# Kernel tuning notes

Hardware: AMD Instinct MI355X
Metric: run time of the kernel (lower is better)

## Reference

```python
import jax, jax.numpy as jnp
import numpy as np

D = 512
H = 8
HD = D // H
EPS = 1e-5
NEG_INF = -1e30


def _ln(x, g, b):
    mu = jnp.mean(x, axis=-1, keepdims=True)
    var = jnp.mean(jnp.square(x - mu), axis=-1, keepdims=True)
    return (x - mu) * jax.lax.rsqrt(var + EPS) * g + b


def setup_inputs() -> dict:
    key = jax.random.key(0)
    ks = jax.random.split(key, 8)
    V, M, S = 128, 128, 514  # seq includes 2 head tokens (cls+dist)
    inp = {
        "video_embeds": jax.random.normal(ks[0], (V, D), jnp.float32),
        "music_features": jax.random.normal(ks[1], (M, S, D), jnp.float32),
        "music_masks": jnp.ones((M, S - 2), jnp.int32),
    }
    wk = jax.random.split(ks[2], 5)
    for name, k in zip(["Wq", "Wk", "Wv", "Wo", "Wl"], wk):
        inp[name] = jax.random.normal(k, (D, D), jnp.float32) * 0.02
    for name in ["bq", "bk", "bv", "bo", "bl"]:
        inp[name] = jnp.zeros((D,), jnp.float32)
    for name in ["g1", "g2", "g3"]:
        inp[name] = jnp.ones((D,), jnp.float32)
    for name in ["b1", "b2", "b3"]:
        inp[name] = jnp.zeros((D,), jnp.float32)
    return inp


def reference(video_embeds, music_features, music_masks,
              Wq, bq, Wk, bk, Wv, bv, Wo, bo, Wl, bl,
              g1, b1, g2, b2, g3, b3):
    # drop cls + dist tokens
    mf = music_features[:, 2:, :]  # (M, f, D)
    ve = _ln(video_embeds, g1, b1)  # (V, D)
    mf = _ln(mf, g1, b1)
    V = ve.shape[0]
    M, f, _ = mf.shape

    q = (ve @ Wq.T + bq).reshape(V, H, HD).transpose(1, 0, 2)        # (H, V, hd)
    k = (mf @ Wk.T + bk).reshape(M, f, H, HD).transpose(0, 2, 1, 3)  # (M, H, f, hd)
    v = (mf @ Wv.T + bv).reshape(M, f, H, HD).transpose(0, 2, 1, 3)  # (M, H, f, hd)

    logits = jnp.einsum('hvd,mhfd->vmhf', q, k) / np.sqrt(HD).astype(np.float32)
    mask = music_masks[None, :, None, :]  # (1, M, 1, f)
    logits = jnp.where(mask == 0, NEG_INF, logits)
    w = jax.nn.softmax(logits, axis=-1)
    attn = jnp.einsum('vmhf,mhfd->vmhd', w, v).reshape(V, M, D)
    attn = attn @ Wo.T + bo

    attn = _ln(attn, g2, b2)
    out = attn + (attn @ Wl.T + bl)  # dropout = identity in eval
    return _ln(out, g3, b3)
```

## Files before the change

### kernel.cpp

```cpp
#include <hip/hip_runtime.h>
#include <hip/hip_bf16.h>

typedef unsigned int uint;
typedef unsigned short ushort;
typedef __bf16 bf16;
typedef bf16 bf16x8 __attribute__((ext_vector_type(8)));
typedef float f32x4 __attribute__((ext_vector_type(4)));
typedef ushort ushort4v __attribute__((ext_vector_type(4)));

__device__ __forceinline__ float bf2f(ushort u) {
  union { uint u; float f; } v; v.u = ((uint)u) << 16; return v.f;
}
__device__ __forceinline__ ushort f2bf(float f) {
  union { float f; uint u; } v; v.f = f;
  uint u = v.u;
  uint r = (u + 0x7fffu + ((u >> 16) & 1u)) >> 16;
  return (ushort)r;
}

__device__ __forceinline__ void gl2lds16(const void* g, void* l) {
  __builtin_amdgcn_global_load_lds(
      (const __attribute__((address_space(1))) void*)g,
      (__attribute__((address_space(3))) void*)l, 16, 0, 0);
}

__device__ __forceinline__ void ln_rows0(
    int nrows, int blk, int nblk, int tid,
    const float* __restrict__ srcA,
    const float* __restrict__ g, const float* __restrict__ b,
    ushort* __restrict__ dst)
{
  const int l = tid & 63;
  const int nw = nblk * 4;
  for (int row = blk * 4 + (tid >> 6); row < nrows; row += nw) {
    const float* s = srcA + (size_t)row * 512;
    float x[8];
    float4 a0 = *(const float4*)(s + l * 4);
    float4 a1 = *(const float4*)(s + 256 + l * 4);
    x[0] = a0.x; x[1] = a0.y; x[2] = a0.z; x[3] = a0.w;
    x[4] = a1.x; x[5] = a1.y; x[6] = a1.z; x[7] = a1.w;
    float sum = 0.f, sq = 0.f;
    #pragma unroll
    for (int j = 0; j < 8; ++j) { sum += x[j]; sq += x[j] * x[j]; }
    #pragma unroll
    for (int o = 1; o < 64; o <<= 1) {
      sum += __shfl_xor(sum, o);
      sq  += __shfl_xor(sq, o);
    }
    float mu = sum * (1.f / 512.f);
    float var = sq * (1.f / 512.f) - mu * mu;
    float rstd = rsqrtf(var + 1e-5f);
    float4 g0 = *(const float4*)(g + l * 4);
    float4 g1 = *(const float4*)(g + 256 + l * 4);
    float4 b0 = *(const float4*)(b + l * 4);
    float4 b1 = *(const float4*)(b + 256 + l * 4);
    float gv[8] = {g0.x,g0.y,g0.z,g0.w,g1.x,g1.y,g1.z,g1.w};
    float bv[8] = {b0.x,b0.y,b0.z,b0.w,b1.x,b1.y,b1.z,b1.w};
    ushort* d = dst + (size_t)row * 512;
    ushort4v p0, p1;
    #pragma unroll
    for (int j = 0; j < 4; ++j) {
      p0[j] = f2bf((x[j] - mu) * rstd * gv[j] + bv[j]);
      p1[j] = f2bf((x[4+j] - mu) * rstd * gv[4+j] + bv[4+j]);
    }
    *(ushort4v*)(d + l * 4) = p0;
    *(ushort4v*)(d + 256 + l * 4) = p1;
  }
}

__device__ __forceinline__ void ln_pair(
    int mode, int wid, int tid,
    const void* __restrict__ srcA, const void* __restrict__ srcB,
    const float* __restrict__ g, const float* __restrict__ b,
    void* __restrict__ dst)
{
  const int l = tid & 63;
  const int r0 = wid * 2, r1 = r0 + 1;
  float x0[8], x1[8];
  if (mode == 1) {
    int mm0 = r0 >> 9, fi0 = r0 & 511;
    int mm1 = r1 >> 9, fi1 = r1 & 511;
    const float* s0 = (const float*)srcA + ((size_t)mm0 * 514 + 2 + fi0) * 512;
    const float* s1 = (const float*)srcA + ((size_t)mm1 * 514 + 2 + fi1) * 512;
    float4 a0 = *(const float4*)(s0 + l * 4);
    float4 a1 = *(const float4*)(s0 + 256 + l * 4);
    float4 c0 = *(const float4*)(s1 + l * 4);
    float4 c1 = *(const float4*)(s1 + 256 + l * 4);
    x0[0]=a0.x; x0[1]=a0.y; x0[2]=a0.z; x0[3]=a0.w;
    x0[4]=a1.x; x0[5]=a1.y; x0[6]=a1.z; x0[7]=a1.w;
    x1[0]=c0.x; x1[1]=c0.y; x1[2]=c0.z; x1[3]=c0.w;
    x1[4]=c1.x; x1[5]=c1.y; x1[6]=c1.z; x1[7]=c1.w;
  } else if (mode == 2) {
    const ushort* s0 = (const ushort*)srcA + (size_t)r0 * 512;
    const ushort* s1 = (const ushort*)srcA + (size_t)r1 * 512;
    uint4 u0 = *(const uint4*)(s0 + l * 8);
    uint4 u1 = *(const uint4*)(s1 + l * 8);
    x0[0]=bf2f((ushort)u0.x); x0[1]=bf2f((ushort)(u0.x>>16));
    x0[2]=bf2f((ushort)u0.y); x0[3]=bf2f((ushort)(u0.y>>16));
    x0[4]=bf2f((ushort)u0.z); x0[5]=bf2f((ushort)(u0.z>>16));
    x0[6]=bf2f((ushort)u0.w); x0[7]=bf2f((ushort)(u0.w>>16));
    x1[0]=bf2f((ushort)u1.x); x1[1]=bf2f((ushort)(u1.x>>16));
    x1[2]=bf2f((ushort)u1.y); x1[3]=bf2f((ushort)(u1.y>>16));
    x1[4]=bf2f((ushort)u1.z); x1[5]=bf2f((ushort)(u1.z>>16));
    x1[6]=bf2f((ushort)u1.w); x1[7]=bf2f((ushort)(u1.w>>16));
  } else {
    const ushort* sa0 = (const ushort*)srcA + (size_t)r0 * 512;
    const ushort* sb0 = (const ushort*)srcB + (size_t)r0 * 512;
    const ushort* sa1 = (const ushort*)srcA + (size_t)r1 * 512;
    const ushort* sb1 = (const ushort*)srcB + (size_t)r1 * 512;
    uint4 ua0 = *(const uint4*)(sa0 + l * 8);
    uint4 ub0 = *(const uint4*)(sb0 + l * 8);
    uint4 ua1 = *(const uint4*)(sa1 + l * 8);
    uint4 ub1 = *(const uint4*)(sb1 + l * 8);
    x0[0]=bf2f((ushort)ua0.x)+bf2f((ushort)ub0.x);
    x0[1]=bf2f((ushort)(ua0.x>>16))+bf2f((ushort)(ub0.x>>16));
    x0[2]=bf2f((ushort)ua0.y)+bf2f((ushort)ub0.y);
    x0[3]=bf2f((ushort)(ua0.y>>16))+bf2f((ushort)(ub0.y>>16));
    x0[4]=bf2f((ushort)ua0.z)+bf2f((ushort)ub0.z);
    x0[5]=bf2f((ushort)(ua0.z>>16))+bf2f((ushort)(ub0.z>>16));
    x0[6]=bf2f((ushort)ua0.w)+bf2f((ushort)ub0.w);
    x0[7]=bf2f((ushort)(ua0.w>>16))+bf2f((ushort)(ub0.w>>16));
    x1[0]=bf2f((ushort)ua1.x)+bf2f((ushort)ub1.x);
    x1[1]=bf2f((ushort)(ua1.x>>16))+bf2f((ushort)(ub1.x>>16));
    x1[2]=bf2f((ushort)ua1.y)+bf2f((ushort)ub1.y);
    x1[3]=bf2f((ushort)(ua1.y>>16))+bf2f((ushort)(ub1.y>>16));
    x1[4]=bf2f((ushort)ua1.z)+bf2f((ushort)ub1.z);
    x1[5]=bf2f((ushort)(ua1.z>>16))+bf2f((ushort)(ub1.z>>16));
    x1[6]=bf2f((ushort)ua1.w)+bf2f((ushort)ub1.w);
    x1[7]=bf2f((ushort)(ua1.w>>16))+bf2f((ushort)(ub1.w>>16));
  }
  float s0 = 0.f, q0 = 0.f, s1 = 0.f, q1 = 0.f;
  #pragma unroll
  for (int j = 0; j < 8; ++j) {
    s0 += x0[j]; q0 += x0[j] * x0[j];
    s1 += x1[j]; q1 += x1[j] * x1[j];
  }
  #pragma unroll
  for (int o = 1; o < 64; o <<= 1) {
    s0 += __shfl_xor(s0, o); q0 += __shfl_xor(q0, o);
    s1 += __shfl_xor(s1, o); q1 += __shfl_xor(q1, o);
  }
  float mu0 = s0 * (1.f/512.f), mu1 = s1 * (1.f/512.f);
  float rstd0 = rsqrtf(q0 * (1.f/512.f) - mu0 * mu0 + 1e-5f);
  float rstd1 = rsqrtf(q1 * (1.f/512.f) - mu1 * mu1 + 1e-5f);

  float gv[8], bv[8];
  if (mode == 1) {
    float4 g0 = *(const float4*)(g + l * 4);
    float4 g1v = *(const float4*)(g + 256 + l * 4);
    float4 b0 = *(const float4*)(b + l * 4);
    float4 b1v = *(const float4*)(b + 256 + l * 4);
    gv[0]=g0.x; gv[1]=g0.y; gv[2]=g0.z; gv[3]=g0.w;
    gv[4]=g1v.x; gv[5]=g1v.y; gv[6]=g1v.z; gv[7]=g1v.w;
    bv[0]=b0.x; bv[1]=b0.y; bv[2]=b0.z; bv[3]=b0.w;
    bv[4]=b1v.x; bv[5]=b1v.y; bv[6]=b1v.z; bv[7]=b1v.w;
  } else {
    float4 g0 = *(const float4*)(g + l * 8);
    float4 g1v = *(const float4*)(g + l * 8 + 4);
    float4 b0 = *(const float4*)(b + l * 8);
    float4 b1v = *(const float4*)(b + l * 8 + 4);
    gv[0]=g0.x; gv[1]=g0.y; gv[2]=g0.z; gv[3]=g0.w;
    gv[4]=g1v.x; gv[5]=g1v.y; gv[6]=g1v.z; gv[7]=g1v.w;
    bv[0]=b0.x; bv[1]=b0.y; bv[2]=b0.z; bv[3]=b0.w;
    bv[4]=b1v.x; bv[5]=b1v.y; bv[6]=b1v.z; bv[7]=b1v.w;
  }
  if (mode == 1) {
    ushort* d0 = (ushort*)dst + (size_t)r0 * 512;
    ushort* d1 = (ushort*)dst + (size_t)r1 * 512;
    ushort4v p00, p01, p10, p11;
    #pragma unroll
    for (int j = 0; j < 4; ++j) {
      p00[j] = f2bf((x0[j]-mu0)*rstd0*gv[j]+bv[j]);
      p01[j] = f2bf((x0[4+j]-mu0)*rstd0*gv[4+j]+bv[4+j]);
      p10[j] = f2bf((x1[j]-mu1)*rstd1*gv[j]+bv[j]);
      p11[j] = f2bf((x1[4+j]-mu1)*rstd1*gv[4+j]+bv[4+j]);
    }
    *(ushort4v*)(d0 + l * 4) = p00;
    *(ushort4v*)(d0 + 256 + l * 4) = p01;
    *(ushort4v*)(d1 + l * 4) = p10;
    *(ushort4v*)(d1 + 256 + l * 4) = p11;
  } else if (mode == 2) {
    ushort* d0 = (ushort*)dst + (size_t)r0 * 512;
    ushort* d1 = (ushort*)dst + (size_t)r1 * 512;
    uint4 o0, o1;
    float y;
    uint t;
    y = (x0[0]-mu0)*rstd0*gv[0]+bv[0]; t = f2bf(y);
    o0.x = t | ((uint)f2bf((x0[1]-mu0)*rstd0*gv[1]+bv[1]) << 16);
    o0.y = (uint)f2bf((x0[2]-mu0)*rstd0*gv[2]+bv[2]) | ((uint)f2bf((x0[3]-mu0)*rstd0*gv[3]+bv[3]) << 16);
    o0.z = (uint)f2bf((x0[4]-mu0)*rstd0*gv[4]+bv[4]) | ((uint)f2bf((x0[5]-mu0)*rstd0*gv[5]+bv[5]) << 16);
    o0.w = (uint)f2bf((x0[6]-mu0)*rstd0*gv[6]+bv[6]) | ((uint)f2bf((x0[7]-mu0)*rstd0*gv[7]+bv[7]) << 16);
    o1.x = (uint)f2bf((x1[0]-mu1)*rstd1*gv[0]+bv[0]) | ((uint)f2bf((x1[1]-mu1)*rstd1*gv[1]+bv[1]) << 16);
    o1.y = (uint)f2bf((x1[2]-mu1)*rstd1*gv[2]+bv[2]) | ((uint)f2bf((x1[3]-mu1)*rstd1*gv[3]+bv[3]) << 16);
    o1.z = (uint)f2bf((x1[4]-mu1)*rstd1*gv[4]+bv[4]) | ((uint)f2bf((x1[5]-mu1)*rstd1*gv[5]+bv[5]) << 16);
    o1.w = (uint)f2bf((x1[6]-mu1)*rstd1*gv[6]+bv[6]) | ((uint)f2bf((x1[7]-mu1)*rstd1*gv[7]+bv[7]) << 16);
    *(uint4*)(d0 + l * 8) = o0;
    *(uint4*)(d1 + l * 8) = o1;
  } else {
    float* d0 = (float*)dst + (size_t)r0 * 512;
    float* d1 = (float*)dst + (size_t)r1 * 512;
    float4 a0, a1, c0, c1;
    a0.x=(x0[0]-mu0)*rstd0*gv[0]+bv[0]; a0.y=(x0[1]-mu0)*rstd0*gv[1]+bv[1];
    a0.z=(x0[2]-mu0)*rstd0*gv[2]+bv[2]; a0.w=(x0[3]-mu0)*rstd0*gv[3]+bv[3];
    a1.x=(x0[4]-mu0)*rstd0*gv[4]+bv[4]; a1.y=(x0[5]-mu0)*rstd0*gv[5]+bv[5];
    a1.z=(x0[6]-mu0)*rstd0*gv[6]+bv[6]; a1.w=(x0[7]-mu0)*rstd0*gv[7]+bv[7];
    c0.x=(x1[0]-mu1)*rstd1*gv[0]+bv[0]; c0.y=(x1[1]-mu1)*rstd1*gv[1]+bv[1];
    c0.z=(x1[2]-mu1)*rstd1*gv[2]+bv[2]; c0.w=(x1[3]-mu1)*rstd1*gv[3]+bv[3];
    c1.x=(x1[4]-mu1)*rstd1*gv[4]+bv[4]; c1.y=(x1[5]-mu1)*rstd1*gv[5]+bv[5];
    c1.z=(x1[6]-mu1)*rstd1*gv[6]+bv[6]; c1.w=(x1[7]-mu1)*rstd1*gv[7]+bv[7];
    *(float4*)(d0 + l * 8) = a0;
    *(float4*)(d0 + l * 8 + 4) = a1;
    *(float4*)(d1 + l * 8) = c0;
    *(float4*)(d1 + l * 8 + 4) = c1;
  }
}

__global__ __launch_bounds__(256) void ln512p(
    int mode, const void* __restrict__ srcA, const void* __restrict__ srcB,
    const float* __restrict__ g, const float* __restrict__ b,
    void* __restrict__ dst)
{
  ln_pair(mode, blockIdx.x * 4 + (threadIdx.x >> 6), threadIdx.x, srcA, srcB, g, b, dst);
}

struct PreArgs {
  const float* s0; const float* s1; const float* s2; const float* s3; const float* s4;
  ushort* d0; ushort* d1; ushort* d2; ushort* d3; ushort* d4;
  const float* video; const float* music;
  const float* g1; const float* b1;
  ushort* veln; ushort* mfln;
};
__global__ __launch_bounds__(256) void preamble(PreArgs a) {
  int bb = blockIdx.x;
  if (bb < 640) {
    int t = bb * 256 + threadIdx.x;
    int which = t >> 15;
    int e = (t & 32767) * 8;
    const float* s = which == 0 ? a.s0 : which == 1 ? a.s1 : which == 2 ? a.s2 : which == 3 ? a.s3 : a.s4;
    ushort*      d = which == 0 ? a.d0 : which == 1 ? a.d1 : which == 2 ? a.d2 : which == 3 ? a.d3 : a.d4;
    float4 v0 = *(const float4*)(s + e);
    float4 v1 = *(const float4*)(s + e + 4);
    uint4 o;
    o.x = (uint)f2bf(v0.x) | ((uint)f2bf(v0.y) << 16);
    o.y = (uint)f2bf(v0.z) | ((uint)f2bf(v0.w) << 16);
    o.z = (uint)f2bf(v1.x) | ((uint)f2bf(v1.y) << 16);
    o.w = (uint)f2bf(v1.z) | ((uint)f2bf(v1.w) << 16);
    *(uint4*)(d + e) = o;
  } else if (bb < 672) {
    ln_rows0(128, bb - 640, 32, threadIdx.x, a.video, a.g1, a.b1, a.veln);
  } else {
    ln_pair(1, (bb - 672) * 4 + (threadIdx.x >> 6), threadIdx.x,
            a.music, nullptr, a.g1, a.b1, a.mfln);
  }
}

__global__ __launch_bounds__(256) void gemm_t3(
    const ushort* __restrict__ A, const ushort* __restrict__ W,
    const float* __restrict__ bias, ushort* __restrict__ C,
    float scale, int vt_mode,
    const ushort* __restrict__ Aq, const ushort* __restrict__ Wqp,
    const float* __restrict__ bqp, ushort* __restrict__ Qout, int qy)
{
  __shared__ __align__(16) ushort As[2][128 * 64];
  __shared__ __align__(16) ushort Bs[2][128 * 64];
  const int tid = threadIdx.x;
  const int w = tid >> 6, l = tid & 63;
  const int lg = l >> 4, lr = l & 15;
  const int wr = w >> 1, wc = w & 1;

  int row0, col0;
  const bool isq = ((int)blockIdx.y == qy);
  if (isq) {
    A = Aq; W = Wqp; bias = bqp; C = Qout; scale = 0.125f; vt_mode = 0;
    row0 = 0; col0 = blockIdx.x * 128;
  } else {
    int nwg = gridDim.x * (qy >= 0 ? qy : gridDim.y);
    int bid = blockIdx.y * gridDim.x + blockIdx.x;
    if ((nwg & 7) == 0) bid = (bid & 7) * (nwg >> 3) + (bid >> 3);
    row0 = (bid / gridDim.x) * 128;
    col0 = (bid % gridDim.x) * 128;
  }

  f32x4 acc[4][4];
  #pragma unroll
  for (int i = 0; i < 4; i++)
    #pragma unroll
    for (int j = 0; j < 4; j++) { f32x4 z = {0.f,0.f,0.f,0.f}; acc[i][j] = z; }

  size_t asrc[4], wsrc[4]; int ldst[4];
  #pragma unroll
  for (int c2 = 0; c2 < 4; ++c2) {
    int c = c2 * 256 + tid;
    int r = c >> 3, j = c & 7;
    int koff = (j ^ (r & 7)) * 8;
    asrc[c2] = (size_t)(row0 + r) * 512 + koff;
    wsrc[c2] = (size_t)(col0 + r) * 512 + koff;
    ldst[c2] = (c2 * 256 + w * 64) * 8;
  }

  auto stage = [&](int pb, int kk) {
    #pragma unroll
    for (int c2 = 0; c2 < 4; ++c2) {
      gl2lds16(A + asrc[c2] + kk * 64, &As[pb][ldst[c2]]);
      gl2lds16(W + wsrc[c2] + kk * 64, &Bs[pb][ldst[c2]]);
    }
  };
  auto compute = [&](int pb) {
    #pragma unroll
    for (int ks = 0; ks < 2; ++ks) {
      bf16x8 af[4], bfr[4];
      #pragma unroll
      for (int mi = 0; mi < 4; ++mi) {
        int r = wr * 64 + mi * 16 + lr;
        af[mi] = *(const bf16x8*)(&As[pb][r * 64 + ((ks * 32 + lg * 8) ^ ((r & 7) * 8))]);
      }
      #pragma unroll
      for (int ni = 0; ni < 4; ++ni) {
        int r = wc * 64 + ni * 16 + lr;
        bfr[ni] = *(const bf16x8*)(&Bs[pb][r * 64 + ((ks * 32 + lg * 8) ^ ((r & 7) * 8))]);
      }
      #pragma unroll
      for (int mi = 0; mi < 4; ++mi)
        #pragma unroll
        for (int ni = 0; ni < 4; ++ni)
          acc[mi][ni] = __builtin_amdgcn_mfma_f32_16x16x32_bf16(af[mi], bfr[ni], acc[mi][ni], 0, 0, 0);
    }
  };

  stage(0, 0);
  __syncthreads();
  int cur = 0;
  #pragma unroll
  for (int kk = 0; kk < 7; ++kk) {
    stage(cur ^ 1, kk + 1);
    compute(cur);
    __syncthreads();
    cur ^= 1;
  }
  compute(cur);
  __syncthreads();

  ushort* img = (ushort*)As;
  #pragma unroll
  for (int ni = 0; ni < 4; ++ni) {
    float bc = bias[col0 + wc * 64 + ni * 16 + lr];
    #pragma unroll
    for (int mi = 0; mi < 4; ++mi) {
      #pragma unroll
      for (int e = 0; e < 4; ++e) {
        float v = (acc[mi][ni][e] + bc) * scale;
        int x, y;
        if (!vt_mode) { x = wr * 64 + mi * 16 + lg * 4 + e; y = wc * 64 + ni * 16 + lr; }
        else          { x = wc * 64 + ni * 16 + lr;         y = wr * 64 + mi * 16 + lg * 4 + e; }
        int byte = x * 256 + ((y * 2) ^ (((x >> 2) & 3) * 32));
        img[byte >> 1] = f2bf(v);
      }
    }
  }
  __syncthreads();
  {
    const int m = row0 >> 9, fi0 = row0 & 511;
    #pragma unroll
    for (int pass = 0; pass < 8; ++pass) {
      int r = pass * 16 + (tid >> 4);
      int cb = tid & 15;
      int byte = r * 256 + ((cb * 16) ^ (((r >> 2) & 3) * 32));
      uint4 d = *(const uint4*)(img + (byte >> 1));
      if (!vt_mode)
        *(uint4*)(C + (size_t)(row0 + r) * 512 + col0 + cb * 8) = d;
      else
        *(uint4*)(C + (size_t)(m * 512 + col0 + r) * 512 + fi0 + cb * 8) = d;
    }
  }
}

__global__ __launch_bounds__(256) void attn_kernel(
    const ushort* __restrict__ q, const ushort* __restrict__ k,
    const ushort* __restrict__ vt, const int* __restrict__ masks,
    ushort* __restrict__ attn)
{
  __shared__ __align__(16) ushort Qs[128 * 64];
  __shared__ __align__(16) ushort Ks[64 * 64];
  __shared__ __align__(16) ushort Vs[64 * 64];
  __shared__ __align__(16) ushort Ps[4][32 * 64];
  __shared__ float maskf[64];
  __shared__ float stats[4][32];

  const int tid = threadIdx.x;
  const int w = tid >> 6, l = tid & 63;
  const int lg = l >> 4, lr = l & 15;
  const int m = blockIdx.x >> 3, h = blockIdx.x & 7;

  const size_t kbase = (size_t)(m * 512) * 512 + h * 64;
  const size_t vbase = (size_t)(m * 512 + h * 64) * 512;

  #pragma unroll
  for (int c2 = 0; c2 < 4; ++c2) {
    int c = c2 * 256 + tid;
    int r = c >> 3, j = c & 7;
    gl2lds16(q + (size_t)r * 512 + h * 64 + ((j * 8) ^ ((r & 7) * 8)),
             Qs + (c2 * 256 + w * 64) * 8);
  }

  f32x4 acc[2][4];
  #pragma unroll
  for (int i = 0; i < 2; i++)
    #pragma unroll
    for (int j = 0; j < 4; j++) { f32x4 z = {0.f,0.f,0.f,0.f}; acc[i][j] = z; }
  float m_run[2] = {-INFINITY, -INFINITY};
  float l_run[2] = {0.f, 0.f};
  bf16x8 qf[2][2];

  for (int it = 0; it < 8; ++it) {
    const int f0 = it * 64;
    #pragma unroll
    for (int c2 = 0; c2 < 2; ++c2) {
      int c = c2 * 256 + tid;
      int r = c >> 3, j = c & 7;
      int off = (j * 8) ^ ((r & 7) * 8);
      gl2lds16(k + kbase + (size_t)(f0 + r) * 512 + off, Ks + (c2 * 256 + w * 64) * 8);
      gl2lds16(vt + vbase + (size_t)r * 512 + f0 + off, Vs + (c2 * 256 + w * 64) * 8);
    }
    if (tid < 64) maskf[tid] = masks[m * 512 + f0 + tid] ? 0.f : -1e30f;
    __syncthreads();

    if (it == 0) {
      #pragma unroll
      for (int nv = 0; nv < 2; ++nv)
        #pragma unroll
        for (int k2 = 0; k2 < 2; ++k2) {
          int v = w * 32 + nv * 16 + lr;
          qf[nv][k2] = *(const bf16x8*)(Qs + v * 64 + ((k2 * 32 + lg * 8) ^ ((v & 7) * 8)));
        }
    }

    f32x4 s[4][2];
    #pragma unroll
    for (int mi = 0; mi < 4; mi++)
      #pragma unroll
      for (int nv = 0; nv < 2; nv++) { f32x4 z = {0.f,0.f,0.f,0.f}; s[mi][nv] = z; }
    #pragma unroll
    for (int k2 = 0; k2 < 2; ++k2) {
      bf16x8 kf[4];
      #pragma unroll
      for (int mi = 0; mi < 4; ++mi) {
        int f = mi * 16 + lr;
        kf[mi] = *(const bf16x8*)(Ks + f * 64 + ((k2 * 32 + lg * 8) ^ ((f & 7) * 8)));
      }
      __builtin_amdgcn_s_setprio(1);
      #pragma unroll
      for (int mi = 0; mi < 4; ++mi)
        #pragma unroll
        for (int nv = 0; nv < 2; ++nv)
          s[mi][nv] = __builtin_amdgcn_mfma_f32_16x16x32_bf16(kf[mi], qf[nv][k2], s[mi][nv], 0, 0, 0);
      __builtin_amdgcn_s_setprio(0);
    }

    float mk[4][4];
    #pragma unroll
    for (int mi = 0; mi < 4; mi++)
      #pragma unroll
      for (int e = 0; e < 4; e++) mk[mi][e] = maskf[mi * 16 + lg * 4 + e];

    #pragma unroll
    for (int nv = 0; nv < 2; ++nv) {
      float cmax = -INFINITY;
      #pragma unroll
      for (int mi = 0; mi < 4; mi++)
        #pragma unroll
        for (int e = 0; e < 4; e++) {
          s[mi][nv][e] += mk[mi][e];
          cmax = fmaxf(cmax, s[mi][nv][e]);
        }
      cmax = fmaxf(cmax, __shfl_xor(cmax, 16));
      cmax = fmaxf(cmax, __shfl_xor(cmax, 32));
      float mnew = fmaxf(m_run[nv], cmax);
      float sc = __expf(m_run[nv] - mnew);
      float csum = 0.f;
      int vloc = nv * 16 + lr;
      #pragma unroll
      for (int mi = 0; mi < 4; mi++) {
        ushort4v pk;
        #pragma unroll
        for (int e = 0; e < 4; e++) {
          float p = __expf(s[mi][nv][e] - mnew);
          csum += p;
          pk[e] = f2bf(p);
        }
        int f = mi * 16 + lg * 4;
        *(ushort4v*)(&Ps[w][vloc * 64 + (f ^ ((vloc & 7) * 8))]) = pk;
      }
      csum += __shfl_xor(csum, 16);
      csum += __shfl_xor(csum, 32);
      l_run[nv] = l_run[nv] * sc + csum;
      m_run[nv] = mnew;
      if (lg == 0) stats[w][vloc] = sc;
    }

    #pragma unroll
    for (int mi2 = 0; mi2 < 2; ++mi2)
      #pragma unroll
      for (int e = 0; e < 4; ++e) {
        float sc = stats[w][mi2 * 16 + lg * 4 + e];
        #pragma unroll
        for (int nd = 0; nd < 4; ++nd) acc[mi2][nd][e] *= sc;
      }

    #pragma unroll
    for (int k2 = 0; k2 < 2; ++k2) {
      bf16x8 pf[2], vf[4];
      #pragma unroll
      for (int mi2 = 0; mi2 < 2; ++mi2) {
        int vloc = mi2 * 16 + lr;
        pf[mi2] = *(const bf16x8*)(&Ps[w][vloc * 64 + ((k2 * 32 + lg * 8) ^ ((vloc & 7) * 8))]);
      }
      #pragma unroll
      for (int nd = 0; nd < 4; ++nd) {
        int d = nd * 16 + lr;
        vf[nd] = *(const bf16x8*)(Vs + d * 64 + ((k2 * 32 + lg * 8) ^ ((d & 7) * 8)));
      }
      __builtin_amdgcn_s_setprio(1);
      #pragma unroll
      for (int mi2 = 0; mi2 < 2; ++mi2)
        #pragma unroll
        for (int nd = 0; nd < 4; ++nd)
          acc[mi2][nd] = __builtin_amdgcn_mfma_f32_16x16x32_bf16(pf[mi2], vf[nd], acc[mi2][nd], 0, 0, 0);
      __builtin_amdgcn_s_setprio(0);
    }
    __syncthreads();
  }

  #pragma unroll
  for (int nv = 0; nv < 2; ++nv)
    if (lg == 0) stats[w][nv * 16 + lr] = 1.f / l_run[nv];
  #pragma unroll
  for (int mi2 = 0; mi2 < 2; ++mi2)
    #pragma unroll
    for (int e = 0; e < 4; ++e) {
      float invl = stats[w][mi2 * 16 + lg * 4 + e];
      int vg = w * 32 + mi2 * 16 + lg * 4 + e;
      #pragma unroll
      for (int nd = 0; nd < 4; ++nd) {
        int d = nd * 16 + lr;
        attn[(size_t)(vg * 128 + m) * 512 + h * 64 + d] = f2bf(acc[mi2][nd][e] * invl);
      }
    }
}

extern "C" void kernel_launch(void* const* d_in, const int* in_sizes, int n_in,
                              void* d_out, int out_size, void* d_ws, size_t ws_size,
                              hipStream_t stream) {
  const float* video = (const float*)d_in[0];
  const float* music = (const float*)d_in[1];
  const int*   masks = (const int*)d_in[2];
  const float* Wq = (const float*)d_in[3];
  const float* Wk = (const float*)d_in[4];
  const float* Wv = (const float*)d_in[5];
  const float* Wo = (const float*)d_in[6];
  const float* Wl = (const float*)d_in[7];
  const float* bq = (const float*)d_in[8];
  const float* bk = (const float*)d_in[9];
  const float* bv = (const float*)d_in[10];
  const float* bo = (const float*)d_in[11];
  const float* bl = (const float*)d_in[12];
  const float* g1 = (const float*)d_in[13];
  const float* g2 = (const float*)d_in[14];
  const float* g3 = (const float*)d_in[15];
  const float* b1 = (const float*)d_in[16];
  const float* b2 = (const float*)d_in[17];
  const float* b3 = (const float*)d_in[18];

  char* ws = (char*)d_ws;
  ushort* mfln = (ushort*)(ws);
  ushort* kbuf = (ushort*)(ws + 67108864);
  ushort* vtb  = (ushort*)(ws + 134217728);
  ushort* attn = (ushort*)(ws + 201326592);
  ushort* c1   = (ushort*)(ws + 218103808);
  ushort* xbuf = (ushort*)(ws + 234881024);
  ushort* veln = (ushort*)(ws + 251658240);
  ushort* qbuf = (ushort*)(ws + 251789312);
  ushort* wqb  = (ushort*)(ws + 251920384);
  ushort* wkb  = wqb + 262144;
  ushort* wvb  = wkb + 262144;
  ushort* wob  = wvb + 262144;
  ushort* wlb  = wob + 262144;

  PreArgs pa = {Wq, Wk, Wv, Wo, Wl, wqb, wkb, wvb, wob, wlb,
                video, music, g1, b1, veln, mfln};
  preamble<<<8864, 256, 0, stream>>>(pa);

  gemm_t3<<<dim3(4, 513), 256, 0, stream>>>(
      mfln, wkb, bk, kbuf, 1.f, 0, veln, wqb, bq, qbuf, 512);
  gemm_t3<<<dim3(4, 512), 256, 0, stream>>>(
      mfln, wvb, bv, vtb, 1.f, 1, nullptr, nullptr, nullptr, nullptr, -1);

  attn_kernel<<<1024, 256, 0, stream>>>(qbuf, kbuf, vtb, masks, attn);

  gemm_t3<<<dim3(4, 128), 256, 0, stream>>>(
      attn, wob, bo, c1, 1.f, 0, nullptr, nullptr, nullptr, nullptr, -1);
  ln512p<<<2048, 256, 0, stream>>>(2, c1, nullptr, g2, b2, xbuf);
  gemm_t3<<<dim3(4, 128), 256, 0, stream>>>(
      xbuf, wlb, bl, c1, 1.f, 0, nullptr, nullptr, nullptr, nullptr, -1);
  ln512p<<<2048, 256, 0, stream>>>(3, xbuf, c1, g3, b3, d_out);
}
```

Before: 328.8 us.

## Rework GEMM into 256x128 triple-buffered tiles and double-buffer attention K/V

The GEMM kernel becomes 512-thread blocks with 256x128 tiles, a three-stage LDS ring buffer driven by explicit vmcnt waits, and MFMA priority hints. The LDS-staged epilogue is dropped in favour of direct global stores, and Q projection is split into its own launch. The attention kernel double-buffers K/V/mask loads so the next tile is prefetched during compute, and it skips the running-max rescale when the new max is within a threshold of the old one. The trade-offs are more LDS per block (lower occupancy), less coalesced direct stores, and an extra kernel launch.

```diff
diff --git a/kernel.cpp b/kernel.cpp
--- a/kernel.cpp
+++ b/kernel.cpp
@@ -183,10 +183,7 @@
     ushort* d0 = (ushort*)dst + (size_t)r0 * 512;
     ushort* d1 = (ushort*)dst + (size_t)r1 * 512;
     uint4 o0, o1;
-    float y;
-    uint t;
-    y = (x0[0]-mu0)*rstd0*gv[0]+bv[0]; t = f2bf(y);
-    o0.x = t | ((uint)f2bf((x0[1]-mu0)*rstd0*gv[1]+bv[1]) << 16);
+    o0.x = (uint)f2bf((x0[0]-mu0)*rstd0*gv[0]+bv[0]) | ((uint)f2bf((x0[1]-mu0)*rstd0*gv[1]+bv[1]) << 16);
     o0.y = (uint)f2bf((x0[2]-mu0)*rstd0*gv[2]+bv[2]) | ((uint)f2bf((x0[3]-mu0)*rstd0*gv[3]+bv[3]) << 16);
     o0.z = (uint)f2bf((x0[4]-mu0)*rstd0*gv[4]+bv[4]) | ((uint)f2bf((x0[5]-mu0)*rstd0*gv[5]+bv[5]) << 16);
     o0.w = (uint)f2bf((x0[6]-mu0)*rstd0*gv[6]+bv[6]) | ((uint)f2bf((x0[7]-mu0)*rstd0*gv[7]+bv[7]) << 16);
@@ -254,32 +251,23 @@
   }
 }
 
-__global__ __launch_bounds__(256) void gemm_t3(
+__global__ __launch_bounds__(512) void gemm_p3(
     const ushort* __restrict__ A, const ushort* __restrict__ W,
     const float* __restrict__ bias, ushort* __restrict__ C,
-    float scale, int vt_mode,
-    const ushort* __restrict__ Aq, const ushort* __restrict__ Wqp,
-    const float* __restrict__ bqp, ushort* __restrict__ Qout, int qy)
+    float scale, int vt_mode, int rowlim)
 {
-  __shared__ __align__(16) ushort As[2][128 * 64];
-  __shared__ __align__(16) ushort Bs[2][128 * 64];
+  __shared__ __align__(16) ushort As[3][256 * 64];
+  __shared__ __align__(16) ushort Bs[3][128 * 64];
   const int tid = threadIdx.x;
   const int w = tid >> 6, l = tid & 63;
   const int lg = l >> 4, lr = l & 15;
   const int wr = w >> 1, wc = w & 1;
 
-  int row0, col0;
-  const bool isq = ((int)blockIdx.y == qy);
-  if (isq) {
-    A = Aq; W = Wqp; bias = bqp; C = Qout; scale = 0.125f; vt_mode = 0;
-    row0 = 0; col0 = blockIdx.x * 128;
-  } else {
-    int nwg = gridDim.x * (qy >= 0 ? qy : gridDim.y);
-    int bid = blockIdx.y * gridDim.x + blockIdx.x;
-    if ((nwg & 7) == 0) bid = (bid & 7) * (nwg >> 3) + (bid >> 3);
-    row0 = (bid / gridDim.x) * 128;
-    col0 = (bid % gridDim.x) * 128;
-  }
+  int nwg = gridDim.x * gridDim.y;
+  int bid = blockIdx.y * gridDim.x + blockIdx.x;
+  if ((nwg & 7) == 0) bid = (bid & 7) * (nwg >> 3) + (bid >> 3);
+  const int bx = bid % gridDim.x, by = bid / gridDim.x;
+  const int row0 = by * 256, col0 = bx * 128;
 
   f32x4 acc[4][4];
   #pragma unroll
@@ -287,23 +275,29 @@
     #pragma unroll
     for (int j = 0; j < 4; j++) { f32x4 z = {0.f,0.f,0.f,0.f}; acc[i][j] = z; }
 
-  size_t asrc[4], wsrc[4]; int ldst[4];
-  #pragma unroll
-  for (int c2 = 0; c2 < 4; ++c2) {
-    int c = c2 * 256 + tid;
-    int r = c >> 3, j = c & 7;
+  size_t asrc[4], wsrc[2]; int aldst[4], wldst[2];
+  {
+    int r = tid >> 3, j = tid & 7;
     int koff = (j ^ (r & 7)) * 8;
-    asrc[c2] = (size_t)(row0 + r) * 512 + koff;
-    wsrc[c2] = (size_t)(col0 + r) * 512 + koff;
-    ldst[c2] = (c2 * 256 + w * 64) * 8;
+    #pragma unroll
+    for (int c2 = 0; c2 < 4; ++c2) {
+      asrc[c2] = (size_t)(row0 + c2 * 64 + r) * 512 + koff;
+      aldst[c2] = ((c2 * 64 + w * 8) * 64);
+    }
+    #pragma unroll
+    for (int c2 = 0; c2 < 2; ++c2) {
+      wsrc[c2] = (size_t)(col0 + c2 * 64 + r) * 512 + koff;
+      wldst[c2] = ((c2 * 64 + w * 8) * 64);
+    }
   }
 
   auto stage = [&](int pb, int kk) {
     #pragma unroll
-    for (int c2 = 0; c2 < 4; ++c2) {
-      gl2lds16(A + asrc[c2] + kk * 64, &As[pb][ldst[c2]]);
-      gl2lds16(W + wsrc[c2] + kk * 64, &Bs[pb][ldst[c2]]);
-    }
+    for (int c2 = 0; c2 < 4; ++c2)
+      gl2lds16(A + asrc[c2] + kk * 64, &As[pb][aldst[c2]]);
+    #pragma unroll
+    for (int c2 = 0; c2 < 2; ++c2)
+      gl2lds16(W + wsrc[c2] + kk * 64, &Bs[pb][wldst[c2]]);
   };
   auto compute = [&](int pb) {
     #pragma unroll
@@ -319,57 +313,53 @@
         int r = wc * 64 + ni * 16 + lr;
         bfr[ni] = *(const bf16x8*)(&Bs[pb][r * 64 + ((ks * 32 + lg * 8) ^ ((r & 7) * 8))]);
       }
+      __builtin_amdgcn_s_setprio(1);
       #pragma unroll
       for (int mi = 0; mi < 4; ++mi)
         #pragma unroll
         for (int ni = 0; ni < 4; ++ni)
           acc[mi][ni] = __builtin_amdgcn_mfma_f32_16x16x32_bf16(af[mi], bfr[ni], acc[mi][ni], 0, 0, 0);
+      __builtin_amdgcn_s_setprio(0);
     }
   };
 
   stage(0, 0);
-  __syncthreads();
-  int cur = 0;
-  #pragma unroll
-  for (int kk = 0; kk < 7; ++kk) {
-    stage(cur ^ 1, kk + 1);
-    compute(cur);
-    __syncthreads();
-    cur ^= 1;
-  }
-  compute(cur);
-  __syncthreads();
-
-  ushort* img = (ushort*)As;
+  stage(1, 1);
+  int cb = 0;
+  for (int t = 0; t < 8; ++t) {
+    if (t < 7) asm volatile("s_waitcnt vmcnt(6)" ::: "memory");
+    else       asm volatile("s_waitcnt vmcnt(0)" ::: "memory");
+    __builtin_amdgcn_s_barrier();
+    __builtin_amdgcn_sched_barrier(0);
+    if (t + 2 < 8) {
+      int nb = cb + 2; if (nb >= 3) nb -= 3;
+      stage(nb, t + 2);
+    }
+    compute(cb);
+    cb = (cb == 2) ? 0 : cb + 1;
+  }
+
   #pragma unroll
   for (int ni = 0; ni < 4; ++ni) {
-    float bc = bias[col0 + wc * 64 + ni * 16 + lr];
+    int cg = col0 + wc * 64 + ni * 16 + lr;
+    float bc = bias[cg];
     #pragma unroll
     for (int mi = 0; mi < 4; ++mi) {
-      #pragma unroll
-      for (int e = 0; e < 4; ++e) {
-        float v = (acc[mi][ni][e] + bc) * scale;
-        int x, y;
-        if (!vt_mode) { x = wr * 64 + mi * 16 + lg * 4 + e; y = wc * 64 + ni * 16 + lr; }
-        else          { x = wc * 64 + ni * 16 + lr;         y = wr * 64 + mi * 16 + lg * 4 + e; }
-        int byte = x * 256 + ((y * 2) ^ (((x >> 2) & 3) * 32));
-        img[byte >> 1] = f2bf(v);
-      }
-    }
-  }
-  __syncthreads();
-  {
-    const int m = row0 >> 9, fi0 = row0 & 511;
-    #pragma unroll
-    for (int pass = 0; pass < 8; ++pass) {
-      int r = pass * 16 + (tid >> 4);
-      int cb = tid & 15;
-      int byte = r * 256 + ((cb * 16) ^ (((r >> 2) & 3) * 32));
-      uint4 d = *(const uint4*)(img + (byte >> 1));
-      if (!vt_mode)
-        *(uint4*)(C + (size_t)(row0 + r) * 512 + col0 + cb * 8) = d;
-      else
-        *(uint4*)(C + (size_t)(m * 512 + col0 + r) * 512 + fi0 + cb * 8) = d;
+      int rg0 = row0 + wr * 64 + mi * 16 + lg * 4;
+      if (rg0 >= rowlim) continue;
+      if (!vt_mode) {
+        #pragma unroll
+        for (int e = 0; e < 4; ++e) {
+          float v = (acc[mi][ni][e] + bc) * scale;
+          C[(size_t)(rg0 + e) * 512 + cg] = f2bf(v);
+        }
+      } else {
+        int m = rg0 >> 9, fi = rg0 & 511;
+        ushort4v pk;
+        #pragma unroll
+        for (int e = 0; e < 4; ++e) pk[e] = f2bf((acc[mi][ni][e] + bc) * scale);
+        *(ushort4v*)(C + (size_t)(m * 512 + cg) * 512 + fi) = pk;
+      }
     }
   }
 }
@@ -380,10 +370,10 @@
     ushort* __restrict__ attn)
 {
   __shared__ __align__(16) ushort Qs[128 * 64];
-  __shared__ __align__(16) ushort Ks[64 * 64];
-  __shared__ __align__(16) ushort Vs[64 * 64];
+  __shared__ __align__(16) ushort Ks[2][64 * 64];
+  __shared__ __align__(16) ushort Vs[2][64 * 64];
   __shared__ __align__(16) ushort Ps[4][32 * 64];
-  __shared__ float maskf[64];
+  __shared__ float maskf[2][64];
   __shared__ float stats[4][32];
 
   const int tid = threadIdx.x;
@@ -393,6 +383,19 @@
 
   const size_t kbase = (size_t)(m * 512) * 512 + h * 64;
   const size_t vbase = (size_t)(m * 512 + h * 64) * 512;
+
+  auto stageKV = [&](int pb, int it) {
+    const int f0 = it * 64;
+    #pragma unroll
+    for (int c2 = 0; c2 < 2; ++c2) {
+      int c = c2 * 256 + tid;
+      int r = c >> 3, j = c & 7;
+      int off = (j * 8) ^ ((r & 7) * 8);
+      gl2lds16(k + kbase + (size_t)(f0 + r) * 512 + off, &Ks[pb][(c2 * 256 + w * 64) * 8]);
+      gl2lds16(vt + vbase + (size_t)r * 512 + f0 + off, &Vs[pb][(c2 * 256 + w * 64) * 8]);
+    }
+    if (tid < 64) maskf[pb][tid] = masks[m * 512 + f0 + tid] ? 0.f : -1e30f;
+  };
 
   #pragma unroll
   for (int c2 = 0; c2 < 4; ++c2) {
@@ -401,6 +404,8 @@
     gl2lds16(q + (size_t)r * 512 + h * 64 + ((j * 8) ^ ((r & 7) * 8)),
              Qs + (c2 * 256 + w * 64) * 8);
   }
+  stageKV(0, 0);
+  __syncthreads();
 
   f32x4 acc[2][4];
   #pragma unroll
@@ -410,29 +415,17 @@
   float m_run[2] = {-INFINITY, -INFINITY};
   float l_run[2] = {0.f, 0.f};
   bf16x8 qf[2][2];
-
+  #pragma unroll
+  for (int nv = 0; nv < 2; ++nv)
+    #pragma unroll
+    for (int k2 = 0; k2 < 2; ++k2) {
+      int v = w * 32 + nv * 16 + lr;
+      qf[nv][k2] = *(const bf16x8*)(Qs + v * 64 + ((k2 * 32 + lg * 8) ^ ((v & 7) * 8)));
+    }
+
+  int cur = 0;
   for (int it = 0; it < 8; ++it) {
-    const int f0 = it * 64;
-    #pragma unroll
-    for (int c2 = 0; c2 < 2; ++c2) {
-      int c = c2 * 256 + tid;
-      int r = c >> 3, j = c & 7;
-      int off = (j * 8) ^ ((r & 7) * 8);
-      gl2lds16(k + kbase + (size_t)(f0 + r) * 512 + off, Ks + (c2 * 256 + w * 64) * 8);
-      gl2lds16(vt + vbase + (size_t)r * 512 + f0 + off, Vs + (c2 * 256 + w * 64) * 8);
-    }
-    if (tid < 64) maskf[tid] = masks[m * 512 + f0 + tid] ? 0.f : -1e30f;
-    __syncthreads();
-
-    if (it == 0) {
-      #pragma unroll
-      for (int nv = 0; nv < 2; ++nv)
-        #pragma unroll
-        for (int k2 = 0; k2 < 2; ++k2) {
-          int v = w * 32 + nv * 16 + lr;
-          qf[nv][k2] = *(const bf16x8*)(Qs + v * 64 + ((k2 * 32 + lg * 8) ^ ((v & 7) * 8)));
-        }
-    }
+    if (it < 7) stageKV(cur ^ 1, it + 1);
 
     f32x4 s[4][2];
     #pragma unroll
@@ -445,7 +438,7 @@
       #pragma unroll
       for (int mi = 0; mi < 4; ++mi) {
         int f = mi * 16 + lr;
-        kf[mi] = *(const bf16x8*)(Ks + f * 64 + ((k2 * 32 + lg * 8) ^ ((f & 7) * 8)));
+        kf[mi] = *(const bf16x8*)(&Ks[cur][f * 64 + ((k2 * 32 + lg * 8) ^ ((f & 7) * 8))]);
       }
       __builtin_amdgcn_s_setprio(1);
       #pragma unroll
@@ -460,22 +453,23 @@
     #pragma unroll
     for (int mi = 0; mi < 4; mi++)
       #pragma unroll
-      for (int e = 0; e < 4; e++) mk[mi][e] = maskf[mi * 16 + lg * 4 + e];
+      for (int e = 0; e < 4; e++) mk[mi][e] = maskf[cur][mi * 16 + lg * 4 + e];
 
     #pragma unroll
     for (int nv = 0; nv < 2; ++nv) {
-      float cmax = -INFINITY;
+      float pmax = -INFINITY;
       #pragma unroll
       for (int mi = 0; mi < 4; mi++)
         #pragma unroll
         for (int e = 0; e < 4; e++) {
           s[mi][nv][e] += mk[mi][e];
-          cmax = fmaxf(cmax, s[mi][nv][e]);
+          pmax = fmaxf(pmax, s[mi][nv][e]);
         }
-      cmax = fmaxf(cmax, __shfl_xor(cmax, 16));
-      cmax = fmaxf(cmax, __shfl_xor(cmax, 32));
-      float mnew = fmaxf(m_run[nv], cmax);
-      float sc = __expf(m_run[nv] - mnew);
+      pmax = fmaxf(pmax, __shfl_xor(pmax, 16));
+      pmax = fmaxf(pmax, __shfl_xor(pmax, 32));
+      bool skip = __all(pmax - m_run[nv] <= 8.f);
+      float mnew = skip ? m_run[nv] : fmaxf(m_run[nv], pmax);
+      float sc = skip ? 1.f : __expf(m_run[nv] - mnew);
       float csum = 0.f;
       int vloc = nv * 16 + lr;
       #pragma unroll
@@ -495,16 +489,16 @@
       l_run[nv] = l_run[nv] * sc + csum;
       m_run[nv] = mnew;
       if (lg == 0) stats[w][vloc] = sc;
-    }
-
-    #pragma unroll
-    for (int mi2 = 0; mi2 < 2; ++mi2)
-      #pragma unroll
-      for (int e = 0; e < 4; ++e) {
-        float sc = stats[w][mi2 * 16 + lg * 4 + e];
-        #pragma unroll
-        for (int nd = 0; nd < 4; ++nd) acc[mi2][nd][e] *= sc;
-      }
+      if (!skip) {
+        int mi2 = nv;
+        #pragma unroll
+        for (int e = 0; e < 4; ++e) {
+          float scv = stats[w][mi2 * 16 + lg * 4 + e];
+          #pragma unroll
+          for (int nd = 0; nd < 4; ++nd) acc[mi2][nd][e] *= scv;
+        }
+      }
+    }
 
     #pragma unroll
     for (int k2 = 0; k2 < 2; ++k2) {
@@ -517,7 +511,7 @@
       #pragma unroll
       for (int nd = 0; nd < 4; ++nd) {
         int d = nd * 16 + lr;
-        vf[nd] = *(const bf16x8*)(Vs + d * 64 + ((k2 * 32 + lg * 8) ^ ((d & 7) * 8)));
+        vf[nd] = *(const bf16x8*)(&Vs[cur][d * 64 + ((k2 * 32 + lg * 8) ^ ((d & 7) * 8))]);
       }
       __builtin_amdgcn_s_setprio(1);
       #pragma unroll
@@ -528,6 +522,7 @@
       __builtin_amdgcn_s_setprio(0);
     }
     __syncthreads();
+    cur ^= 1;
   }
 
   #pragma unroll
@@ -589,17 +584,14 @@
                 video, music, g1, b1, veln, mfln};
   preamble<<<8864, 256, 0, stream>>>(pa);
 
-  gemm_t3<<<dim3(4, 513), 256, 0, stream>>>(
-      mfln, wkb, bk, kbuf, 1.f, 0, veln, wqb, bq, qbuf, 512);
-  gemm_t3<<<dim3(4, 512), 256, 0, stream>>>(
-      mfln, wvb, bv, vtb, 1.f, 1, nullptr, nullptr, nullptr, nullptr, -1);
+  gemm_p3<<<dim3(4, 1), 512, 0, stream>>>(veln, wqb, bq, qbuf, 0.125f, 0, 128);
+  gemm_p3<<<dim3(4, 256), 512, 0, stream>>>(mfln, wkb, bk, kbuf, 1.f, 0, 1 << 30);
+  gemm_p3<<<dim3(4, 256), 512, 0, stream>>>(mfln, wvb, bv, vtb, 1.f, 1, 1 << 30);
 
   attn_kernel<<<1024, 256, 0, stream>>>(qbuf, kbuf, vtb, masks, attn);
 
-  gemm_t3<<<dim3(4, 128), 256, 0, stream>>>(
-      attn, wob, bo, c1, 1.f, 0, nullptr, nullptr, nullptr, nullptr, -1);
+  gemm_p3<<<dim3(4, 64), 512, 0, stream>>>(attn, wob, bo, c1, 1.f, 0, 1 << 30);
   ln512p<<<2048, 256, 0, stream>>>(2, c1, nullptr, g2, b2, xbuf);
-  gemm_t3<<<dim3(4, 128), 256, 0, stream>>>(
-      xbuf, wlb, bl, c1, 1.f, 0, nullptr, nullptr, nullptr, nullptr, -1);
+  gemm_p3<<<dim3(4, 64), 512, 0, stream>>>(xbuf, wlb, bl, c1, 1.f, 0, 1 << 30);
   ln512p<<<2048, 256, 0, stream>>>(3, xbuf, c1, g3, b3, d_out);
 }
```

After: 291.8 us. 1.13x faster.
